# Kernel optimization log

Hardware: AMD Instinct MI355X
Metric: run time of the kernel (lower is better)

The kernel has to match this reference:

```python
import jax, jax.numpy as jnp
import numpy as np

# ---- static configuration (mirrors init_kwargs) ----
B, V, C, NH, HD = 1, 6, 256, 8, 32     # batch, views, embed, heads, head_dim
Z, L, P = 4, 4, 2                       # z-ref points, fmap levels, ref points
BEV_H, BEV_W = 80, 80
Q = BEV_H * BEV_W
IMG_H, IMG_W = 480, 800
LEVEL_SHAPES = [(60, 100), (30, 50), (15, 25), (8, 13)]
S = sum(h * w for h, w in LEVEL_SHAPES)
RES = 0.512
OFFSET_SCALE = 1.0
FF = 512


def layer_norm(x, g, b):
    m = jnp.mean(x, -1, keepdims=True)
    v = jnp.var(x, -1, keepdims=True)
    return (x - m) / jnp.sqrt(v + 1e-5) * g + b


def _bev_grid():
    xs = (jnp.arange(BEV_W) + 0.5) / BEV_W
    ys = (jnp.arange(BEV_H) + 0.5) / BEV_H
    gy, gx = jnp.meshgrid(ys, xs, indexing='ij')
    ref = jnp.stack([gx.reshape(-1), gy.reshape(-1)], -1)        # (Q,2) normalized xy
    world = (ref - 0.5) * jnp.array([BEV_W * RES, BEV_H * RES])  # (Q,2) ego-frame meters
    return ref, world


def deform_sample(value, H, W, loc):
    """Bilinear sampling. value: (N, H*W, NH, HD); loc: (N, Qn, NH, PP, 2) in [0,1].
    Returns (N, Qn, NH, PP, HD); out-of-bounds samples contribute zero."""
    v = jnp.moveaxis(value, 2, 1)                                # (N, NH, HW, HD)
    x = loc[..., 0] * W - 0.5
    y = loc[..., 1] * H - 0.5
    x0 = jnp.floor(x); y0 = jnp.floor(y)
    lx, ly = x - x0, y - y0
    x0 = x0.astype(jnp.int32); y0 = y0.astype(jnp.int32)
    gather = jax.vmap(jax.vmap(lambda vt, it: vt[it]))           # over (N, NH)
    def corner(xi, yi, w):
        ok = ((xi >= 0) & (xi < W) & (yi >= 0) & (yi < H)).astype(value.dtype)
        idx = jnp.clip(yi, 0, H - 1) * W + jnp.clip(xi, 0, W - 1)
        g = gather(v, jnp.moveaxis(idx, 2, 1))                   # (N,NH,Qn,PP,HD)
        return jnp.moveaxis(g, 1, 2) * (w * ok)[..., None]
    return (corner(x0, y0, (1 - lx) * (1 - ly)) + corner(x0 + 1, y0, lx * (1 - ly))
            + corner(x0, y0 + 1, (1 - lx) * ly) + corner(x0 + 1, y0 + 1, lx * ly))


def _forward(bev_queries, bev_histories, multiscale_fmaps, transition_matrices, z_refs,
             cam_proj_matrices, Wv_t, Woff_t, boff_t, Ww_t, bw_t, Wo_t, bo_t, ln1_g, ln1_b,
             Wv_s, Woff_s, boff_s, Ww_s, bw_s, Wo_s, bo_s, ln2_g, ln2_b,
             W1, b1, W2, b2, ln3_g, ln3_b):
    ref, world = _bev_grid()
    q = bev_queries
    # ---------- temporal self-attention (deformable over current + warped history) ----------
    vcur = (q @ Wv_t).reshape(B, Q, NH, HD)
    vhist = (bev_histories @ Wv_t).reshape(B, Q, NH, HD)
    off_t = (q @ Woff_t + boff_t).reshape(B, Q, NH, 2, P, 2) * OFFSET_SCALE
    w_t = jax.nn.softmax((q @ Ww_t + bw_t).reshape(B, Q, NH, 2 * P), -1).reshape(B, Q, NH, 2, P)
    ext = jnp.array([BEV_W * RES, BEV_H * RES], jnp.float32)
    wh = jnp.concatenate([world, jnp.ones((Q, 1), jnp.float32)], -1)     # (Q,3)
    warped = jnp.einsum('bij,qj->bqi', transition_matrices, wh)          # (B,Q,3)
    ref_hist = warped[..., :2] / warped[..., 2:3] / ext + 0.5            # (B,Q,2)
    norm_bev = jnp.array([BEV_W, BEV_H], jnp.float32)
    loc_c = ref[None, :, None, None, :] + off_t[:, :, :, 0] / norm_bev
    loc_h = ref_hist[:, :, None, None, :] + off_t[:, :, :, 1] / norm_bev
    s_c = deform_sample(vcur, BEV_H, BEV_W, loc_c)                       # (B,Q,NH,P,HD)
    s_h = deform_sample(vhist, BEV_H, BEV_W, loc_h)
    out_t = (jnp.einsum('bqhp,bqhpd->bqhd', w_t[:, :, :, 0], s_c)
             + jnp.einsum('bqhp,bqhpd->bqhd', w_t[:, :, :, 1], s_h))
    out1 = out_t.reshape(B, Q, C) @ Wo_t + bo_t
    out2 = layer_norm(out1 + q, ln1_g, ln1_b)
    # ---------- spatial cross-attention (multi-view multi-scale deformable) ----------
    val = (multiscale_fmaps @ Wv_s).reshape(B * V, S, NH, HD)
    pts = jnp.concatenate([
        jnp.broadcast_to(world[:, None, :], (Q, Z, 2)),
        jnp.broadcast_to(z_refs[None, :, None], (Q, Z, 1)),
        jnp.ones((Q, Z, 1), jnp.float32)], -1)                           # (Q,Z,4) homogeneous
    uvd = jnp.einsum('vij,qzj->vqzi', cam_proj_matrices, pts)            # (V,Q,Z,3)
    d = uvd[..., 2]
    un = uvd[..., 0] / jnp.maximum(d, 1e-5) / IMG_W
    vn = uvd[..., 1] / jnp.maximum(d, 1e-5) / IMG_H
    valid = ((d > 1e-5) & (un >= 0) & (un <= 1) & (vn >= 0) & (vn <= 1)).astype(q.dtype)
    refuv = jnp.stack([un, vn], -1)                                      # (V,Q,Z,2)
    off_s = (out2 @ Woff_s + boff_s).reshape(B, Q, NH, Z, L, P, 2) * OFFSET_SCALE
    w_s = jax.nn.softmax((out2 @ Ww_s + bw_s).reshape(B, Q, NH, Z * L * P), -1)
    w_s = w_s.reshape(B, Q, NH, Z, L, P)
    acc = jnp.zeros((B, Q, NH, HD), q.dtype)
    start = 0
    for l, (Hl, Wl) in enumerate(LEVEL_SHAPES):
        vl = val[:, start:start + Hl * Wl]
        start += Hl * Wl
        loc = (refuv[None, :, :, None, :, None, :]
               + off_s[:, None, :, :, :, l] / jnp.array([Wl, Hl], jnp.float32))
        loc = jnp.broadcast_to(loc, (B, V, Q, NH, Z, P, 2)).reshape(B * V, Q, NH, Z * P, 2)
        samp = deform_sample(vl, Hl, Wl, loc).reshape(B, V, Q, NH, Z, P, HD)
        wl = w_s[:, None, :, :, :, l] * valid[None, :, :, None, :, None]
        acc = acc + jnp.einsum('bvqhzp,bvqhzpd->bqhd', wl, samp)
    count = jnp.maximum(valid.sum((0, 2)), 1.0)                          # (Q,) hit count
    out3 = (acc / count[None, :, None, None]).reshape(B, Q, C) @ Wo_s + bo_s
    out4 = layer_norm(out3 + out2, ln2_g, ln2_b)
    # ---------- feed-forward ----------
    out5 = jax.nn.relu(out4 @ W1 + b1) @ W2 + b2
    return layer_norm(out5 + out4, ln3_g, ln3_b)


def setup_inputs() -> dict:
    key = jax.random.key(0)
    ks = iter(jax.random.split(key, 40))
    def rn(shape, s=1.0):
        return jax.random.normal(next(ks), shape, jnp.float32) * s
    sc = 1.0 / float(np.sqrt(C))
    inp = {}
    inp['bev_queries'] = rn((B, Q, C), 0.1)
    inp['bev_histories'] = rn((B, Q, C), 0.1)
    inp['multiscale_fmaps'] = rn((B, V, S, C), 0.1)
    th = 0.02
    T = np.array([[np.cos(th), -np.sin(th), 0.5],
                  [np.sin(th), np.cos(th), 0.1],
                  [0.0, 0.0, 1.0]], np.float32)
    inp['transition_matrices'] = jnp.tile(jnp.asarray(T)[None], (B, 1, 1))
    inp['z_refs'] = jnp.linspace(-5.0, 3.0, Z).astype(jnp.float32)
    K = np.array([[400.0, 0.0, IMG_W / 2], [0.0, 400.0, IMG_H / 2], [0.0, 0.0, 1.0]], np.float32)
    Ps = []
    for vi in range(V):
        a = 2 * np.pi * vi / V
        Rt = np.zeros((3, 4), np.float32)
        Rt[0, :3] = [-np.sin(a), np.cos(a), 0.0]   # camera right
        Rt[1, :3] = [0.0, 0.0, -1.0]               # camera down
        Rt[2, :3] = [np.cos(a), np.sin(a), 0.0]    # camera forward
        Ps.append(K @ Rt)
    inp['cam_proj_matrices'] = jnp.asarray(np.stack(Ps))
    # temporal self-attention params
    inp['Wv_t'] = rn((C, C), sc)
    inp['Woff_t'] = rn((C, NH * 2 * P * 2), sc * 0.1)
    inp['boff_t'] = jnp.zeros((NH * 2 * P * 2,), jnp.float32)
    inp['Ww_t'] = rn((C, NH * 2 * P), sc)
    inp['bw_t'] = jnp.zeros((NH * 2 * P,), jnp.float32)
    inp['Wo_t'] = rn((C, C), sc)
    inp['bo_t'] = jnp.zeros((C,), jnp.float32)
    inp['ln1_g'] = jnp.ones((C,), jnp.float32)
    inp['ln1_b'] = jnp.zeros((C,), jnp.float32)
    # spatial cross-attention params
    inp['Wv_s'] = rn((C, C), sc)
    inp['Woff_s'] = rn((C, NH * Z * L * P * 2), sc * 0.1)
    inp['boff_s'] = jnp.zeros((NH * Z * L * P * 2,), jnp.float32)
    inp['Ww_s'] = rn((C, NH * Z * L * P), sc)
    inp['bw_s'] = jnp.zeros((NH * Z * L * P,), jnp.float32)
    inp['Wo_s'] = rn((C, C), sc)
    inp['bo_s'] = jnp.zeros((C,), jnp.float32)
    inp['ln2_g'] = jnp.ones((C,), jnp.float32)
    inp['ln2_b'] = jnp.zeros((C,), jnp.float32)
    # FFN params
    inp['W1'] = rn((C, FF), sc)
    inp['b1'] = jnp.zeros((FF,), jnp.float32)
    inp['W2'] = rn((FF, C), 1.0 / float(np.sqrt(FF)))
    inp['b2'] = jnp.zeros((C,), jnp.float32)
    inp['ln3_g'] = jnp.ones((C,), jnp.float32)
    inp['ln3_b'] = jnp.zeros((C,), jnp.float32)
    # static shape descriptors (treated as compile-time constants)
    inp['bev_spatial_shape'] = np.array([[BEV_H, BEV_W]], np.int64)
    inp['multiscale_fmap_shapes'] = np.array(LEVEL_SHAPES, np.int64)
    inp['img_spatial_shape'] = np.array([[IMG_H, IMG_W]], np.int64)
    return inp


def reference(bev_queries, bev_histories, multiscale_fmaps, transition_matrices, z_refs,
              cam_proj_matrices, Wv_t, Woff_t, boff_t, Ww_t, bw_t, Wo_t, bo_t, ln1_g, ln1_b,
              Wv_s, Woff_s, boff_s, Ww_s, bw_s, Wo_s, bo_s, ln2_g, ln2_b,
              W1, b1, W2, b2, ln3_g, ln3_b,
              bev_spatial_shape, multiscale_fmap_shapes, img_spatial_shape):
    return _forward(bev_queries, bev_histories, multiscale_fmaps, transition_matrices, z_refs,
                    cam_proj_matrices, Wv_t, Woff_t, boff_t, Ww_t, bw_t, Wo_t, bo_t, ln1_g, ln1_b,
                    Wv_s, Woff_s, boff_s, Ww_s, bw_s, Wo_s, bo_s, ln2_g, ln2_b,
                    W1, b1, W2, b2, ln3_g, ln3_b)
```

## Files before the change

### kernel.cpp

```cpp
#include <hip/hip_runtime.h>
#include <hip/hip_bf16.h>
#include <hip/hip_fp16.h>

typedef unsigned short u16;
typedef unsigned int u32;
typedef __attribute__((ext_vector_type(8))) _Float16 f16x8;
typedef __attribute__((ext_vector_type(4))) float f32x4;

#define Q_N  6400
#define S_N  7979
#define BEV  80

__device__ __forceinline__ float f16tof(u16 u) {
    __half h; *(u16*)&h = u; return __half2float(h);
}
__device__ __forceinline__ u16 ftof16(float f) {
    __half h = __float2half(f); return *(u16*)&h;
}

template <int AIN, int RELU, int OUTMODE, int SM4, int SM32>
__device__ __forceinline__ void gemm_body(
    const void* __restrict__ A, const u16* __restrict__ WT,
    const float* __restrict__ bias, const float* __restrict__ bias2,
    void* __restrict__ Cout, int M, int N, int K, int bx, int by,
    u16* Ah, u16* Wh)
{
    const int tid  = threadIdx.x;
    const int lane = tid & 63;
    const int wave = tid >> 6;
    const int wm = (wave >> 1) * 32, wn = (wave & 1) * 64;
    const int m0 = by * 64, n0 = bx * 128;
    const int arow = tid >> 2, ak = (tid & 3) * 8;
    const int wrow = tid >> 1, wk = (tid & 1) * 16;
    const int fr = lane & 15, g = lane >> 4;

    f32x4 acc[8];
    #pragma unroll
    for (int i = 0; i < 8; ++i) acc[i] = (f32x4)(0.f);

    for (int k0 = 0; k0 < K; k0 += 32) {
        {
            const bool okr = (m0 + arow) < M;
            u16* dh = &Ah[arow * 40 + ak];
            if (AIN == 0) {
                const float* ap = (const float*)A + (size_t)(m0 + arow) * K + k0 + ak;
                float4 v0 = okr ? *(const float4*)(ap)     : make_float4(0.f, 0.f, 0.f, 0.f);
                float4 v1 = okr ? *(const float4*)(ap + 4) : make_float4(0.f, 0.f, 0.f, 0.f);
                u16 hb[8];
                hb[0] = ftof16(v0.x); hb[1] = ftof16(v0.y);
                hb[2] = ftof16(v0.z); hb[3] = ftof16(v0.w);
                hb[4] = ftof16(v1.x); hb[5] = ftof16(v1.y);
                hb[6] = ftof16(v1.z); hb[7] = ftof16(v1.w);
                *(ushort4*)(dh)     = *(ushort4*)&hb[0];
                *(ushort4*)(dh + 4) = *(ushort4*)&hb[4];
            } else {
                const u16* ap = (const u16*)A + (size_t)(m0 + arow) * K + k0 + ak;
                uint4 u = okr ? *(const uint4*)ap : make_uint4(0, 0, 0, 0);
                *(uint4*)dh = u;
            }
        }
        {
            const size_t wo = (size_t)(n0 + wrow) * K + k0 + wk;
            *(uint4*)&Wh[wrow * 40 + wk]     = *(const uint4*)(WT + wo);
            *(uint4*)&Wh[wrow * 40 + wk + 8] = *(const uint4*)(WT + wo + 8);
        }
        __syncthreads();
        f16x8 fah[2], fwh[4];
        #pragma unroll
        for (int i = 0; i < 2; ++i)
            fah[i] = *(const f16x8*)&Ah[(wm + i * 16 + fr) * 40 + g * 8];
        #pragma unroll
        for (int j = 0; j < 4; ++j)
            fwh[j] = *(const f16x8*)&Wh[(wn + j * 16 + fr) * 40 + g * 8];
        #pragma unroll
        for (int i = 0; i < 2; ++i)
            #pragma unroll
            for (int j = 0; j < 4; ++j)
                acc[i * 4 + j] = __builtin_amdgcn_mfma_f32_16x16x32_f16(fah[i], fwh[j], acc[i * 4 + j], 0, 0, 0);
        __syncthreads();
    }
    const int g4r = g * 4;
    float bv[4];
    #pragma unroll
    for (int j = 0; j < 4; ++j) {
        int col = n0 + wn + j * 16 + fr;
        if (bias2) bv[j] = (col < 512) ? bias[col] : bias2[col - 512];
        else       bv[j] = bias ? bias[col] : 0.f;
    }
    const bool do_sm4  = SM4 && (wn == 64);
    #pragma unroll
    for (int i = 0; i < 2; ++i) {
        #pragma unroll
        for (int r = 0; r < 4; ++r) {
            const int row = m0 + wm + i * 16 + g4r + r;
            float v0 = acc[i * 4 + 0][r] + bv[0];
            float v1 = acc[i * 4 + 1][r] + bv[1];
            float v2 = acc[i * 4 + 2][r] + bv[2];
            float v3 = acc[i * 4 + 3][r] + bv[3];
            if (RELU) {
                v0 = fmaxf(v0, 0.f); v1 = fmaxf(v1, 0.f);
                v2 = fmaxf(v2, 0.f); v3 = fmaxf(v3, 0.f);
            }
            if (SM4 && do_sm4) {
                float m0q = fmaxf(v0, __shfl_xor(v0, 1));
                m0q = fmaxf(m0q, __shfl_xor(m0q, 2));
                float e0 = __expf(v0 - m0q);
                float s0 = e0 + __shfl_xor(e0, 1);
                s0 += __shfl_xor(s0, 2);
                v0 = e0 / s0;
                float m1q = fmaxf(v1, __shfl_xor(v1, 1));
                m1q = fmaxf(m1q, __shfl_xor(m1q, 2));
                float e1 = __expf(v1 - m1q);
                float s1 = e1 + __shfl_xor(e1, 1);
                s1 += __shfl_xor(s1, 2);
                v1 = e1 / s1;
                v2 = 0.f; v3 = 0.f;
            }
            if (row < M) {
                const int colb = n0 + wn + fr;
                if (OUTMODE == 1) {
                    u16* cp = (u16*)Cout + (size_t)row * N;
                    cp[colb]      = ftof16(v0);
                    cp[colb + 16] = ftof16(v1);
                    cp[colb + 32] = ftof16(v2);
                    cp[colb + 48] = ftof16(v3);
                } else {
                    float* cp = (float*)Cout + (size_t)row * N;
                    cp[colb]      = v0;
                    cp[colb + 16] = v1;
                    cp[colb + 32] = v2;
                    cp[colb + 48] = v3;
                }
            }
        }
    }
}

__global__ __launch_bounds__(256) void fused3_k(
    const float* __restrict__ fmaps, const float* __restrict__ q, const float* __restrict__ hist,
    const u16* __restrict__ Wv_s_h, const u16* __restrict__ Wv_t_h,
    const u16* __restrict__ Wc_h, const float* __restrict__ bc,
    u16* __restrict__ val_f16, u16* __restrict__ vcur, u16* __restrict__ vhist,
    float* __restrict__ owt)
{
    __shared__ u16 Ah[64 * 40], Wh[128 * 40];
    const int b = blockIdx.x;
    if (b < 1498) {
        gemm_body<0, 0, 1, 0, 0>(fmaps, Wv_s_h, nullptr, nullptr, val_f16,
                                 47874, 256, 256, b & 1, b >> 1, Ah, Wh);
    } else if (b < 1698) {
        int l = b - 1498;
        gemm_body<0, 0, 1, 0, 0>(q, Wv_t_h, nullptr, nullptr, vcur,
                                 6400, 256, 256, l & 1, l >> 1, Ah, Wh);
    } else if (b < 1898) {
        int l = b - 1698;
        gemm_body<0, 0, 1, 0, 0>(hist, Wv_t_h, nullptr, nullptr, vhist,
                                 6400, 256, 256, l & 1, l >> 1, Ah, Wh);
    } else {
        int l = b - 1898;
        gemm_body<0, 0, 0, 1, 0>(q, Wc_h, bc, nullptr, owt,
                                 6400, 128, 256, 0, l, Ah, Wh);
    }
}

template <int AIN, int RELU, int OUTMODE, int SM32>
__global__ __launch_bounds__(256, 4) void cgemm_k(
    const void* __restrict__ A, const u16* __restrict__ WT,
    const float* __restrict__ bias, const float* __restrict__ bias2,
    void* __restrict__ Cout, int M, int N, int K)
{
    __shared__ u16 As[2][32 * 40];
    __shared__ u16 Wsh[2][64 * 40];
    const int tid  = threadIdx.x;
    const int lane = tid & 63;
    const int wave = tid >> 6;
    const int wm = (wave >> 1) * 16, wn = (wave & 1) * 32;
    const int fr = lane & 15, g = lane >> 4;
    const int nx = gridDim.x;
    const int nwg = nx * gridDim.y;
    const int o = blockIdx.y * nx + blockIdx.x;
    const int flat = (o & 7) * (nwg >> 3) + (o >> 3);
    const int bx = flat % nx, by = flat / nx;
    const int m0 = by * 32, n0 = bx * 64;
    const int ar = tid >> 3, ak = (tid & 7) * 4;
    const int wr = tid >> 2, wk = (tid & 3) * 8;
    const int NS = K >> 5;

    f32x4 acc[2] = {(f32x4)(0.f), (f32x4)(0.f)};

    const float* apf = (const float*)A + (size_t)(m0 + ar) * K + ak;
    const u16*  aph  = (const u16*)A + (size_t)(m0 + ar) * K + ak;
    const u16*  wp   = WT + (size_t)(n0 + wr) * K + wk;

    if (AIN == 0) {
        float4 v = *(const float4*)apf;
        u16 hb[4];
        hb[0] = ftof16(v.x); hb[1] = ftof16(v.y); hb[2] = ftof16(v.z); hb[3] = ftof16(v.w);
        *(ushort4*)&As[0][ar * 40 + ak] = *(ushort4*)&hb[0];
    } else {
        *(uint2*)&As[0][ar * 40 + ak] = *(const uint2*)aph;
    }
    *(uint4*)&Wsh[0][wr * 40 + wk] = *(const uint4*)wp;
    __syncthreads();

    for (int s = 0; s < NS; ++s) {
        float4 av; uint2 au; uint4 wv;
        const bool pf = (s + 1) < NS;
        if (pf) {
            if (AIN == 0) av = *(const float4*)(apf + (s + 1) * 32);
            else          au = *(const uint2*)(aph + (s + 1) * 32);
            wv = *(const uint4*)(wp + (s + 1) * 32);
        }
        const int b = s & 1;
        f16x8 fa  = *(const f16x8*)&As[b][(wm + fr) * 40 + g * 8];
        f16x8 fw0 = *(const f16x8*)&Wsh[b][(wn + fr) * 40 + g * 8];
        f16x8 fw1 = *(const f16x8*)&Wsh[b][(wn + 16 + fr) * 40 + g * 8];
        acc[0] = __builtin_amdgcn_mfma_f32_16x16x32_f16(fa, fw0, acc[0], 0, 0, 0);
        acc[1] = __builtin_amdgcn_mfma_f32_16x16x32_f16(fa, fw1, acc[1], 0, 0, 0);
        if (pf) {
            const int nb = b ^ 1;
            if (AIN == 0) {
                u16 hb[4];
                hb[0] = ftof16(av.x); hb[1] = ftof16(av.y);
                hb[2] = ftof16(av.z); hb[3] = ftof16(av.w);
                *(ushort4*)&As[nb][ar * 40 + ak] = *(ushort4*)&hb[0];
            } else {
                *(uint2*)&As[nb][ar * 40 + ak] = au;
            }
            *(uint4*)&Wsh[nb][wr * 40 + wk] = wv;
        }
        __syncthreads();
    }

    const int c0g = n0 + wn + fr, c1g = c0g + 16;
    float bv0, bv1;
    if (bias2) {
        bv0 = (c0g < 512) ? bias[c0g] : bias2[c0g - 512];
        bv1 = (c1g < 512) ? bias[c1g] : bias2[c1g - 512];
    } else {
        bv0 = bias ? bias[c0g] : 0.f;
        bv1 = bias ? bias[c1g] : 0.f;
    }
    const bool do_sm32 = SM32 && ((n0 + wn) >= 512);
    #pragma unroll
    for (int r = 0; r < 4; ++r) {
        const int row = m0 + wm + g * 4 + r;
        float v0 = acc[0][r] + bv0;
        float v1 = acc[1][r] + bv1;
        if (RELU) { v0 = fmaxf(v0, 0.f); v1 = fmaxf(v1, 0.f); }
        if (SM32 && do_sm32) {
            float ma = fmaxf(v0, v1);
            ma = fmaxf(ma, __shfl_xor(ma, 1));
            ma = fmaxf(ma, __shfl_xor(ma, 2));
            ma = fmaxf(ma, __shfl_xor(ma, 4));
            ma = fmaxf(ma, __shfl_xor(ma, 8));
            float e0 = __expf(v0 - ma), e1 = __expf(v1 - ma);
            float sa = e0 + e1;
            sa += __shfl_xor(sa, 1);
            sa += __shfl_xor(sa, 2);
            sa += __shfl_xor(sa, 4);
            sa += __shfl_xor(sa, 8);
            float ia = 1.f / sa;
            v0 = e0 * ia; v1 = e1 * ia;
        }
        if (row < M) {
            if (OUTMODE == 1) {
                u16* cp = (u16*)Cout + (size_t)row * N;
                cp[c0g] = ftof16(v0);
                cp[c1g] = ftof16(v1);
            } else {
                float* cp = (float*)Cout + (size_t)row * N;
                cp[c0g] = v0;
                cp[c1g] = v1;
            }
        }
    }
}

__global__ __launch_bounds__(256) void wprep_k(
    const float* __restrict__ w0, const float* __restrict__ w1, const float* __restrict__ w2,
    const float* __restrict__ w3, const float* __restrict__ w4, const float* __restrict__ w5,
    const float* __restrict__ w6, const float* __restrict__ w7, u16* __restrict__ base,
    const float* __restrict__ Woff_t, const float* __restrict__ Ww_t,
    const float* __restrict__ boff_t, const float* __restrict__ bw_t,
    float* __restrict__ bc)
{
    const int b = blockIdx.x, tid = threadIdx.x;
    if (b == 184) {
        if (tid < 128) bc[tid] = (tid < 64) ? boff_t[tid] : (tid < 96 ? bw_t[tid - 64] : 0.f);
        return;
    }
    const int cum[10]  = {0, 16, 32, 48, 80, 96, 112, 144, 176, 184};
    const int Ks[9]    = {256, 256, 256, 256, 256, 256, 256, 512, 256};
    const int Ns[9]    = {256, 256, 256, 512, 256, 256, 512, 256, 128};
    const int hoff[9]  = {0, 65536, 131072, 196608, 327680, 393216, 458752, 589824, 720896};
    int seg = 0;
    #pragma unroll
    for (int s = 1; s < 9; ++s) if (b >= cum[s]) seg = s;
    const int K = Ks[seg], N = Ns[seg];
    const int t = b - cum[seg];
    const int ntn = N / 64;
    const int k0 = (t / ntn) * 64, n0 = (t % ntn) * 64;
    __shared__ float tile[64][65];
    const int rr = tid >> 2, cc = (tid & 3) * 16;
    if (seg < 8) {
        const float* W = seg == 0 ? w0 : seg == 1 ? w1 : seg == 2 ? w2 : seg == 3 ? w3 :
                         seg == 4 ? w4 : seg == 5 ? w5 : seg == 6 ? w6 : w7;
        #pragma unroll
        for (int c = 0; c < 4; ++c) {
            float4 v = *(const float4*)(W + (size_t)(k0 + rr) * N + n0 + cc + c * 4);
            tile[rr][cc + c * 4 + 0] = v.x;
            tile[rr][cc + c * 4 + 1] = v.y;
            tile[rr][cc + c * 4 + 2] = v.z;
            tile[rr][cc + c * 4 + 3] = v.w;
        }
    } else {
        #pragma unroll
        for (int i = 0; i < 16; ++i) {
            int n = n0 + cc + i, k = k0 + rr;
            float v = (n < 64) ? Woff_t[k * 64 + n] : (n < 96 ? Ww_t[k * 32 + n - 64] : 0.f);
            tile[rr][cc + i] = v;
        }
    }
    __syncthreads();
    const int nr = tid >> 2, kc = (tid & 3) * 16;
    u16 hb[16];
    #pragma unroll
    for (int i = 0; i < 16; ++i) hb[i] = ftof16(tile[kc + i][nr]);
    u16* hp = base + hoff[seg] + (size_t)(n0 + nr) * K + k0 + kc;
    *(ushort4*)(hp + 0)  = *(ushort4*)&hb[0];
    *(ushort4*)(hp + 4)  = *(ushort4*)&hb[4];
    *(ushort4*)(hp + 8)  = *(ushort4*)&hb[8];
    *(ushort4*)(hp + 12) = *(ushort4*)&hb[12];
}

__global__ __launch_bounds__(256) void ln_k(
    const float* __restrict__ x, const float* __restrict__ res,
    const float* __restrict__ g, const float* __restrict__ b,
    float* __restrict__ out)
{
    const int row = blockIdx.x, t = threadIdx.x;
    const size_t idx = (size_t)row * 256 + t;
    float v = x[idx] + res[idx];
    float s = v, ss = v * v;
    #pragma unroll
    for (int o = 32; o > 0; o >>= 1) {
        s += __shfl_down(s, o);
        ss += __shfl_down(ss, o);
    }
    __shared__ float red[8];
    __shared__ float mv[2];
    const int wv = t >> 6, ln = t & 63;
    if (ln == 0) { red[wv] = s; red[4 + wv] = ss; }
    __syncthreads();
    if (t == 0) {
        float S = red[0] + red[1] + red[2] + red[3];
        float SS = red[4] + red[5] + red[6] + red[7];
        float mean = S * (1.f / 256.f);
        float var = SS * (1.f / 256.f) - mean * mean;
        mv[0] = mean;
        mv[1] = rsqrtf(var + 1e-5f);
    }
    __syncthreads();
    out[idx] = (v - mv[0]) * mv[1] * g[t] + b[t];
}

__device__ __forceinline__ float4 bilin4h(const u16* __restrict__ v, int H, int W,
                                          float x, float y, int chb)
{
    float xf = floorf(x), yf = floorf(y);
    int x0 = (int)xf, y0 = (int)yf;
    int x1 = x0 + 1, y1 = y0 + 1;
    float fx = x - xf, fy = y - yf;
    float w00 = (1.f - fx) * (1.f - fy), w10 = fx * (1.f - fy);
    float w01 = (1.f - fx) * fy,         w11 = fx * fy;
    bool xi0 = (x0 >= 0) && (x0 < W);
    bool xi1 = (x1 >= 0) && (x1 < W);
    bool yi0 = (y0 >= 0) && (y0 < H);
    bool yi1 = (y1 >= 0) && (y1 < H);
    float4 r = make_float4(0.f, 0.f, 0.f, 0.f);
    #define CORNER(xi, yi, xx, yy, ww)                                           \
        if ((yi) && (xi)) {                                                      \
            uint2 u = *(const uint2*)(v + ((size_t)(yy) * W + (xx)) * 256 + chb);\
            float2 f0 = __half22float2(*(const __half2*)&u.x);                   \
            float2 f1 = __half22float2(*(const __half2*)&u.y);                   \
            r.x += (ww) * f0.x; r.y += (ww) * f0.y;                              \
            r.z += (ww) * f1.x; r.w += (ww) * f1.y;                              \
        }
    CORNER(xi0, yi0, x0, y0, w00)
    CORNER(xi1, yi0, x1, y0, w10)
    CORNER(xi0, yi1, x0, y1, w01)
    CORNER(xi1, yi1, x1, y1, w11)
    #undef CORNER
    return r;
}

__global__ __launch_bounds__(256) void temporal_k(
    const u16* __restrict__ vcur, const u16* __restrict__ vhist,
    const float* __restrict__ ow,
    const float* __restrict__ Tm, float* __restrict__ outt)
{
    const int b = blockIdx.x;
    const int q = (b & 7) * 800 + (b >> 3);
    const int tid = threadIdx.x;
    const int c4 = tid & 63, rep = tid >> 6;
    const int br = rep >> 1, p = rep & 1;
    const int h = c4 >> 3;
    const int chb = h * 32 + (c4 & 7) * 4;
    const int jx = q % BEV, iy = q / BEV;
    const float refx = (jx + 0.5f) / 80.f;
    const float refy = (iy + 0.5f) / 80.f;
    const float wx = (refx - 0.5f) * 40.96f;
    const float wy = (refy - 0.5f) * 40.96f;
    float bx, by;
    const u16* v;
    if (br == 0) { v = vcur; bx = refx; by = refy; }
    else {
        float h0 = Tm[0] * wx + Tm[1] * wy + Tm[2];
        float h1 = Tm[3] * wx + Tm[4] * wy + Tm[5];
        float h2 = Tm[6] * wx + Tm[7] * wy + Tm[8];
        v = vhist;
        bx = h0 / h2 / 40.96f + 0.5f;
        by = h1 / h2 / 40.96f + 0.5f;
    }
    const float* owq = ow + (size_t)q * 128;
    int ob = h * 8 + br * 4 + p * 2;
    float lx = bx + owq[ob] * (1.f / 80.f);
    float ly = by + owq[ob + 1] * (1.f / 80.f);
    float wgt = owq[64 + h * 4 + br * 2 + p];
    float4 sv = bilin4h(v, BEV, BEV, lx * 80.f - 0.5f, ly * 80.f - 0.5f, chb);
    __shared__ float4 s_acc[4][64];
    s_acc[rep][c4] = make_float4(wgt * sv.x, wgt * sv.y, wgt * sv.z, wgt * sv.w);
    __syncthreads();
    if (rep == 0) {
        float4 a = s_acc[0][c4], b2 = s_acc[1][c4], c = s_acc[2][c4], d = s_acc[3][c4];
        float4 o = make_float4(a.x + b2.x + c.x + d.x, a.y + b2.y + c.y + d.y,
                               a.z + b2.z + c.z + d.z, a.w + b2.w + c.w + d.w);
        *(float4*)(outt + (size_t)q * 256 + c4 * 4) = o;
    }
}

__global__ __launch_bounds__(256) void spatial_k(
    const u16* __restrict__ val, const u16* __restrict__ ow,
    const float* __restrict__ cam, const float* __restrict__ zrefs,
    float* __restrict__ out)
{
    const int b = blockIdx.x;
    const int q = (b & 7) * 800 + (b >> 3);
    const int tid = threadIdx.x;
    const int lane = tid & 63, wave = tid >> 6;
    const int hw = lane >> 5, lh = lane & 31;
    const int slot = wave * 2 + hw;
    const int h = lh >> 2, chb = h * 32 + (lh & 3) * 8;
    __shared__ float s_un[24], s_vn[24], s_ok[24];
    __shared__ int s_list[24];
    __shared__ int s_n;
    __shared__ float s_cnt;
    __shared__ float s_ox[256], s_oy[256], s_wt[256];
    __shared__ float s_part[8][256];
    const int jx = q % BEV, iy = q / BEV;
    const float wx = ((jx + 0.5f) / 80.f - 0.5f) * 40.96f;
    const float wy = ((iy + 0.5f) / 80.f - 0.5f) * 40.96f;
    if (tid < 24) {
        int v = tid >> 2, zz = tid & 3;
        float zr = zrefs[zz];
        const float* P = cam + v * 12;
        float u0 = P[0] * wx + P[1] * wy + P[2] * zr + P[3];
        float u1 = P[4] * wx + P[5] * wy + P[6] * zr + P[7];
        float dd = P[8] * wx + P[9] * wy + P[10] * zr + P[11];
        float dm = fmaxf(dd, 1e-5f);
        float un = u0 / dm / 800.f;
        float vn = u1 / dm / 480.f;
        bool ok = (dd > 1e-5f) && (un >= 0.f) && (un <= 1.f) && (vn >= 0.f) && (vn <= 1.f);
        s_un[tid] = un; s_vn[tid] = vn; s_ok[tid] = ok ? 1.f : 0.f;
    }
    {
        const u16* owq = ow + (size_t)q * 768;
        #pragma unroll
        for (int rep = 0; rep < 2; ++rep) {
            int flat = tid + rep * 256;
            int hh = flat >> 6, rem = flat & 63;
            int zz = rem >> 4, ll = (rem >> 2) & 3, pp = (rem >> 1) & 1, xy = rem & 1;
            int dst = (zz * 8 + ll * 2 + pp) * 8 + hh;
            float v = f16tof(owq[flat]);
            if (xy) s_oy[dst] = v; else s_ox[dst] = v;
        }
        int hh = tid >> 5, rem = tid & 31;
        s_wt[rem * 8 + hh] = f16tof(owq[512 + tid]);
    }
    __syncthreads();
    if (tid == 0) {
        int n = 0; float c = 0.f;
        for (int vz = 0; vz < 24; ++vz) {
            if (s_ok[vz] != 0.f) { s_list[n++] = vz; c += 1.f; }
        }
        s_n = n; s_cnt = fmaxf(c, 1.f);
    }
    __syncthreads();
    const int n4 = s_n * 4;
    float a0 = 0.f, a1 = 0.f, a2 = 0.f, a3 = 0.f, a4 = 0.f, a5 = 0.f, a6 = 0.f, a7 = 0.f;
    for (int w = slot; w < n4; w += 8) {
        const int it = w >> 2, l = w & 3;
        const int vz = s_list[it];
        const int v = vz >> 2, z = vz & 3;
        const float un = s_un[vz], vn = s_vn[vz];
        const int Hl  = (l == 0) ? 60  : (l == 1) ? 30   : (l == 2) ? 15   : 8;
        const int Wl  = (l == 0) ? 100 : (l == 1) ? 50   : (l == 2) ? 25   : 13;
        const int LSo = (l == 0) ? 0   : (l == 1) ? 6000 : (l == 2) ? 7500 : 7875;
        const u16* lv = val + ((size_t)v * S_N + LSo) * 256 + chb;
        const float unl = un * Wl - 0.5f, vnl = vn * Hl - 0.5f;
        const int Ws = Wl * 256;
        #pragma unroll
        for (int p = 0; p < 2; ++p) {
            const int idx = (z * 8 + l * 2 + p) * 8 + h;
            float x = unl + s_ox[idx];
            float y = vnl + s_oy[idx];
            float wgt = s_wt[idx];
            float xf = floorf(x), yf = floorf(y);
            int x0 = (int)xf, y0 = (int)yf;
            float fx = x - xf, fy = y - yf;
            bool xi0 = (x0 >= 0) & (x0 < Wl);
            bool xi1 = (x0 >= -1) & (x0 < Wl - 1);
            bool yi0 = (y0 >= 0) & (y0 < Hl);
            bool yi1 = (y0 >= -1) & (y0 < Hl - 1);
            int xc0 = min(max(x0, 0), Wl - 1);
            int xc1 = min(max(x0 + 1, 0), Wl - 1);
            int yc0 = min(max(y0, 0), Hl - 1);
            int yc1 = min(max(y0 + 1, 0), Hl - 1);
            float m00 = (xi0 & yi0) ? wgt : 0.f;
            float m10 = (xi1 & yi0) ? wgt : 0.f;
            float m01 = (xi0 & yi1) ? wgt : 0.f;
            float m11 = (xi1 & yi1) ? wgt : 0.f;
            __half2 w00 = __float2half2_rn((1.f - fx) * (1.f - fy) * m00);
            __half2 w10 = __float2half2_rn(fx * (1.f - fy) * m10);
            __half2 w01 = __float2half2_rn((1.f - fx) * fy * m01);
            __half2 w11 = __float2half2_rn(fx * fy * m11);
            const u16* r0p = lv + (size_t)yc0 * Ws;
            const u16* r1p = lv + (size_t)yc1 * Ws;
            uint4 u00 = *(const uint4*)(r0p + (size_t)xc0 * 256);
            uint4 u10 = *(const uint4*)(r0p + (size_t)xc1 * 256);
            uint4 u01 = *(const uint4*)(r1p + (size_t)xc0 * 256);
            uint4 u11 = *(const uint4*)(r1p + (size_t)xc1 * 256);
            __half2 h0 = __float2half2_rn(0.f), h1 = h0, h2 = h0, h3 = h0;
            {
                const __half2* hp = (const __half2*)&u00;
                h0 = __hfma2(w00, hp[0], h0); h1 = __hfma2(w00, hp[1], h1);
                h2 = __hfma2(w00, hp[2], h2); h3 = __hfma2(w00, hp[3], h3);
            }
            {
                const __half2* hp = (const __half2*)&u10;
                h0 = __hfma2(w10, hp[0], h0); h1 = __hfma2(w10, hp[1], h1);
                h2 = __hfma2(w10, hp[2], h2); h3 = __hfma2(w10, hp[3], h3);
            }
            {
                const __half2* hp = (const __half2*)&u01;
                h0 = __hfma2(w01, hp[0], h0); h1 = __hfma2(w01, hp[1], h1);
                h2 = __hfma2(w01, hp[2], h2); h3 = __hfma2(w01, hp[3], h3);
            }
            {
                const __half2* hp = (const __half2*)&u11;
                h0 = __hfma2(w11, hp[0], h0); h1 = __hfma2(w11, hp[1], h1);
                h2 = __hfma2(w11, hp[2], h2); h3 = __hfma2(w11, hp[3], h3);
            }
            float2 f0 = __half22float2(h0), f1 = __half22float2(h1);
            float2 f2 = __half22float2(h2), f3 = __half22float2(h3);
            a0 += f0.x; a1 += f0.y; a2 += f1.x; a3 += f1.y;
            a4 += f2.x; a5 += f2.y; a6 += f3.x; a7 += f3.y;
        }
    }
    *(float4*)&s_part[slot][chb]     = make_float4(a0, a1, a2, a3);
    *(float4*)&s_part[slot][chb + 4] = make_float4(a4, a5, a6, a7);
    __syncthreads();
    float sum = 0.f;
    #pragma unroll
    for (int k = 0; k < 8; ++k) sum += s_part[k][tid];
    out[(size_t)q * 256 + tid] = sum / s_cnt;
}

extern "C" void kernel_launch(void* const* d_in, const int* in_sizes, int n_in,
                              void* d_out, int out_size, void* d_ws, size_t ws_size,
                              hipStream_t stream) {
    (void)in_sizes; (void)n_in; (void)out_size; (void)ws_size;
    const float* q      = (const float*)d_in[0];
    const float* hist   = (const float*)d_in[1];
    const float* fmaps  = (const float*)d_in[2];
    const float* Tm     = (const float*)d_in[3];
    const float* zrefs  = (const float*)d_in[4];
    const float* cam    = (const float*)d_in[5];
    const float* Woff_t = (const float*)d_in[7];
    const float* boff_t = (const float*)d_in[8];
    const float* Ww_t   = (const float*)d_in[9];
    const float* bw_t   = (const float*)d_in[10];
    const float* bo_t   = (const float*)d_in[12];
    const float* ln1g   = (const float*)d_in[13];
    const float* ln1b   = (const float*)d_in[14];
    const float* boff_s = (const float*)d_in[17];
    const float* bw_s   = (const float*)d_in[19];
    const float* bo_s   = (const float*)d_in[21];
    const float* ln2g   = (const float*)d_in[22];
    const float* ln2b   = (const float*)d_in[23];
    const float* b1     = (const float*)d_in[25];
    const float* b2     = (const float*)d_in[27];
    const float* ln3g   = (const float*)d_in[28];
    const float* ln3b   = (const float*)d_in[29];

    float* ws    = (float*)d_ws;
    float* r0    = ws;
    float* r1    = ws + 1638400;
    float* owt   = ws + 3276800;
    float* r4    = ws + 4096000;
    u16*  r5u    = (u16*)(ws + 5734400);
    float* of4   = ws + 8192000;
    u16*  valbuf = (u16*)(ws + 9830400);
    u16*  vcur   = (u16*)(ws + 15958272);
    u16*  vhist  = (u16*)(ws + 16777472);
    u16*  wtab   = (u16*)(ws + 17596672);
    float* bc    = ws + 18350336;

    u16* hidden = valbuf;
    u16* Wv_t_h = wtab + 0;
    u16* Wo_t_h = wtab + 65536;
    u16* Wv_s_h = wtab + 131072;
    u16* Comb_h = wtab + 196608;
    u16* Wo_s_h = wtab + 393216;
    u16* W1_h   = wtab + 458752;
    u16* W2_h   = wtab + 589824;
    u16* Wc_h   = wtab + 720896;

    dim3 blk(256);
    auto gc = [](int M, int N) { return dim3((unsigned)(N / 64), (unsigned)((M + 31) / 32)); };

    wprep_k<<<dim3(185), blk, 0, stream>>>(
        (const float*)d_in[6], (const float*)d_in[11], (const float*)d_in[15],
        (const float*)d_in[16], (const float*)d_in[18], (const float*)d_in[20],
        (const float*)d_in[24], (const float*)d_in[26], wtab,
        Woff_t, Ww_t, boff_t, bw_t, bc);
    fused3_k<<<dim3(1998), blk, 0, stream>>>(
        fmaps, q, hist, Wv_s_h, Wv_t_h, Wc_h, bc,
        valbuf, vcur, vhist, owt);
    temporal_k<<<dim3(6400), blk, 0, stream>>>(vcur, vhist, owt, Tm, r4);
    cgemm_k<0,0,0,0><<<gc(6400, 256), blk, 0, stream>>>(
        r4, Wo_t_h, bo_t, nullptr, r0, 6400, 256, 256);
    ln_k<<<dim3(6400), blk, 0, stream>>>(r0, q, ln1g, ln1b, r1);
    cgemm_k<0,0,1,1><<<gc(6400, 768), blk, 0, stream>>>(
        r1, Comb_h, boff_s, bw_s, r5u, 6400, 768, 256);
    spatial_k<<<dim3(6400), blk, 0, stream>>>(valbuf, r5u, cam, zrefs, r0);
    cgemm_k<0,0,0,0><<<gc(6400, 256), blk, 0, stream>>>(
        r0, Wo_s_h, bo_s, nullptr, r4, 6400, 256, 256);
    ln_k<<<dim3(6400), blk, 0, stream>>>(r4, r1, ln2g, ln2b, of4);
    cgemm_k<0,1,1,0><<<gc(6400, 512), blk, 0, stream>>>(
        of4, W1_h, b1, nullptr, hidden, 6400, 512, 256);
    cgemm_k<1,0,0,0><<<gc(6400, 256), blk, 0, stream>>>(
        hidden, W2_h, b2, nullptr, r0, 6400, 256, 512);
    ln_k<<<dim3(6400), blk, 0, stream>>>(r0, of4, ln3g, ln3b, (float*)d_out);
}
```

Measured before the change: 304.4 us.

## Double-buffer GEMM LDS tiles and widen spatial sampling per-thread channels

```diff
diff --git a/kernel.cpp b/kernel.cpp
--- a/kernel.cpp
+++ b/kernel.cpp
@@ -33,50 +33,85 @@
     const int arow = tid >> 2, ak = (tid & 3) * 8;
     const int wrow = tid >> 1, wk = (tid & 1) * 16;
     const int fr = lane & 15, g = lane >> 4;
+    const int NS = K >> 5;
+
+    const bool okr = (m0 + arow) < M;
+    const float* apf = (const float*)A + (size_t)(m0 + arow) * K + ak;
+    const u16*  aph  = (const u16*)A + (size_t)(m0 + arow) * K + ak;
+    const u16*  wp   = WT + (size_t)(n0 + wrow) * K + wk;
 
     f32x4 acc[8];
     #pragma unroll
     for (int i = 0; i < 8; ++i) acc[i] = (f32x4)(0.f);
 
-    for (int k0 = 0; k0 < K; k0 += 32) {
-        {
-            const bool okr = (m0 + arow) < M;
-            u16* dh = &Ah[arow * 40 + ak];
+    {
+        u16* dh = &Ah[arow * 40 + ak];
+        if (AIN == 0) {
+            float4 v0 = okr ? *(const float4*)(apf)     : make_float4(0.f, 0.f, 0.f, 0.f);
+            float4 v1 = okr ? *(const float4*)(apf + 4) : make_float4(0.f, 0.f, 0.f, 0.f);
+            u16 hb[8];
+            hb[0] = ftof16(v0.x); hb[1] = ftof16(v0.y);
+            hb[2] = ftof16(v0.z); hb[3] = ftof16(v0.w);
+            hb[4] = ftof16(v1.x); hb[5] = ftof16(v1.y);
+            hb[6] = ftof16(v1.z); hb[7] = ftof16(v1.w);
+            *(ushort4*)(dh)     = *(ushort4*)&hb[0];
+            *(ushort4*)(dh + 4) = *(ushort4*)&hb[4];
+        } else {
+            uint4 u = okr ? *(const uint4*)aph : make_uint4(0, 0, 0, 0);
+            *(uint4*)dh = u;
+        }
+        *(uint4*)&Wh[wrow * 40 + wk]     = *(const uint4*)(wp);
+        *(uint4*)&Wh[wrow * 40 + wk + 8] = *(const uint4*)(wp + 8);
+    }
+    __syncthreads();
+
+    for (int s = 0; s < NS; ++s) {
+        float4 av0, av1; uint4 au; uint4 wv0, wv1;
+        const bool pf = (s + 1) < NS;
+        if (pf) {
             if (AIN == 0) {
-                const float* ap = (const float*)A + (size_t)(m0 + arow) * K + k0 + ak;
-                float4 v0 = okr ? *(const float4*)(ap)     : make_float4(0.f, 0.f, 0.f, 0.f);
-                float4 v1 = okr ? *(const float4*)(ap + 4) : make_float4(0.f, 0.f, 0.f, 0.f);
-                u16 hb[8];
-                hb[0] = ftof16(v0.x); hb[1] = ftof16(v0.y);
-                hb[2] = ftof16(v0.z); hb[3] = ftof16(v0.w);
-                hb[4] = ftof16(v1.x); hb[5] = ftof16(v1.y);
-                hb[6] = ftof16(v1.z); hb[7] = ftof16(v1.w);
-                *(ushort4*)(dh)     = *(ushort4*)&hb[0];
-                *(ushort4*)(dh + 4) = *(ushort4*)&hb[4];
+                av0 = okr ? *(const float4*)(apf + (s + 1) * 32)     : make_float4(0.f, 0.f, 0.f, 0.f);
+                av1 = okr ? *(const float4*)(apf + (s + 1) * 32 + 4) : make_float4(0.f, 0.f, 0.f, 0.f);
             } else {
-                const u16* ap = (const u16*)A + (size_t)(m0 + arow) * K + k0 + ak;
-                uint4 u = okr ? *(const uint4*)ap : make_uint4(0, 0, 0, 0);
-                *(uint4*)dh = u;
-            }
-        }
-        {
-            const size_t wo = (size_t)(n0 + wrow) * K + k0 + wk;
-            *(uint4*)&Wh[wrow * 40 + wk]     = *(const uint4*)(WT + wo);
-            *(uint4*)&Wh[wrow * 40 + wk + 8] = *(const uint4*)(WT + wo + 8);
-        }
-        __syncthreads();
+                au = okr ? *(const uint4*)(aph + (s + 1) * 32) : make_uint4(0, 0, 0, 0);
+            }
+            wv0 = *(const uint4*)(wp + (s + 1) * 32);
+            wv1 = *(const uint4*)(wp + (s + 1) * 32 + 8);
+        }
+        const int b = s & 1;
+        const u16* Ab = Ah + b * 2560;
+        const u16* Wb = Wh + b * 5120;
         f16x8 fah[2], fwh[4];
         #pragma unroll
         for (int i = 0; i < 2; ++i)
-            fah[i] = *(const f16x8*)&Ah[(wm + i * 16 + fr) * 40 + g * 8];
+            fah[i] = *(const f16x8*)&Ab[(wm + i * 16 + fr) * 40 + g * 8];
         #pragma unroll
         for (int j = 0; j < 4; ++j)
-            fwh[j] = *(const f16x8*)&Wh[(wn + j * 16 + fr) * 40 + g * 8];
+            fwh[j] = *(const f16x8*)&Wb[(wn + j * 16 + fr) * 40 + g * 8];
         #pragma unroll
         for (int i = 0; i < 2; ++i)
             #pragma unroll
             for (int j = 0; j < 4; ++j)
                 acc[i * 4 + j] = __builtin_amdgcn_mfma_f32_16x16x32_f16(fah[i], fwh[j], acc[i * 4 + j], 0, 0, 0);
+        if (pf) {
+            const int nb = b ^ 1;
+            u16* Anb = Ah + nb * 2560;
+            u16* Wnb = Wh + nb * 5120;
+            u16* dh = &Anb[arow * 40 + ak];
+            if (AIN == 0) {
+                u16 hb[8];
+                hb[0] = ftof16(av0.x); hb[1] = ftof16(av0.y);
+                hb[2] = ftof16(av0.z); hb[3] = ftof16(av0.w);
+                hb[4] = ftof16(av1.x); hb[5] = ftof16(av1.y);
+                hb[6] = ftof16(av1.z); hb[7] = ftof16(av1.w);
+                *(ushort4*)(dh)     = *(ushort4*)&hb[0];
+                *(ushort4*)(dh + 4) = *(ushort4*)&hb[4];
+            } else {
+                *(uint4*)dh = au;
+            }
+            *(uint4*)&Wnb[wrow * 40 + wk]     = wv0;
+            *(uint4*)&Wnb[wrow * 40 + wk + 8] = wv1;
+        }
         __syncthreads();
     }
     const int g4r = g * 4;
@@ -143,7 +178,7 @@
     u16* __restrict__ val_f16, u16* __restrict__ vcur, u16* __restrict__ vhist,
     float* __restrict__ owt)
 {
-    __shared__ u16 Ah[64 * 40], Wh[128 * 40];
+    __shared__ u16 Ah[2 * 64 * 40], Wh[2 * 128 * 40];
     const int b = blockIdx.x;
     if (b < 1498) {
         gemm_body<0, 0, 1, 0, 0>(fmaps, Wv_s_h, nullptr, nullptr, val_f16,
@@ -449,15 +484,15 @@
     const int q = (b & 7) * 800 + (b >> 3);
     const int tid = threadIdx.x;
     const int lane = tid & 63, wave = tid >> 6;
-    const int hw = lane >> 5, lh = lane & 31;
-    const int slot = wave * 2 + hw;
-    const int h = lh >> 2, chb = h * 32 + (lh & 3) * 8;
+    const int qw = lane >> 4, lh = lane & 15;
+    const int slot = wave * 4 + qw;
+    const int h = lh >> 1, chb = h * 32 + (lh & 1) * 16;
     __shared__ float s_un[24], s_vn[24], s_ok[24];
     __shared__ int s_list[24];
     __shared__ int s_n;
     __shared__ float s_cnt;
     __shared__ float s_ox[256], s_oy[256], s_wt[256];
-    __shared__ float s_part[8][256];
+    __shared__ float s_part[16][256];
     const int jx = q % BEV, iy = q / BEV;
     const float wx = ((jx + 0.5f) / 80.f - 0.5f) * 40.96f;
     const float wy = ((iy + 0.5f) / 80.f - 0.5f) * 40.96f;
@@ -498,8 +533,10 @@
     }
     __syncthreads();
     const int n4 = s_n * 4;
-    float a0 = 0.f, a1 = 0.f, a2 = 0.f, a3 = 0.f, a4 = 0.f, a5 = 0.f, a6 = 0.f, a7 = 0.f;
-    for (int w = slot; w < n4; w += 8) {
+    float acc[16];
+    #pragma unroll
+    for (int i = 0; i < 16; ++i) acc[i] = 0.f;
+    for (int w = slot; w < n4; w += 16) {
         const int it = w >> 2, l = w & 3;
         const int vz = s_list[it];
         const int v = vz >> 2, z = vz & 3;
@@ -537,43 +574,73 @@
             __half2 w11 = __float2half2_rn(fx * fy * m11);
             const u16* r0p = lv + (size_t)yc0 * Ws;
             const u16* r1p = lv + (size_t)yc1 * Ws;
-            uint4 u00 = *(const uint4*)(r0p + (size_t)xc0 * 256);
-            uint4 u10 = *(const uint4*)(r0p + (size_t)xc1 * 256);
-            uint4 u01 = *(const uint4*)(r1p + (size_t)xc0 * 256);
-            uint4 u11 = *(const uint4*)(r1p + (size_t)xc1 * 256);
-            __half2 h0 = __float2half2_rn(0.f), h1 = h0, h2 = h0, h3 = h0;
+            const u16* c00 = r0p + (size_t)xc0 * 256;
+            const u16* c10 = r0p + (size_t)xc1 * 256;
+            const u16* c01 = r1p + (size_t)xc0 * 256;
+            const u16* c11 = r1p + (size_t)xc1 * 256;
+            uint4 a00 = *(const uint4*)(c00);
+            uint4 b00 = *(const uint4*)(c00 + 8);
+            uint4 a10 = *(const uint4*)(c10);
+            uint4 b10 = *(const uint4*)(c10 + 8);
+            uint4 a01 = *(const uint4*)(c01);
+            uint4 b01 = *(const uint4*)(c01 + 8);
+            uint4 a11 = *(const uint4*)(c11);
+            uint4 b11 = *(const uint4*)(c11 + 8);
+            __half2 t[8];
+            #pragma unroll
+            for (int i = 0; i < 8; ++i) t[i] = __float2half2_rn(0.f);
             {
-                const __half2* hp = (const __half2*)&u00;
-                h0 = __hfma2(w00, hp[0], h0); h1 = __hfma2(w00, hp[1], h1);
-                h2 = __hfma2(w00, hp[2], h2); h3 = __hfma2(w00, hp[3], h3);
+                const __half2* hp = (const __half2*)&a00;
+                const __half2* hq = (const __half2*)&b00;
+                #pragma unroll
+                for (int i = 0; i < 4; ++i) {
+                    t[i]     = __hfma2(w00, hp[i], t[i]);
+                    t[i + 4] = __hfma2(w00, hq[i], t[i + 4]);
+                }
             }
             {
-                const __half2* hp = (const __half2*)&u10;
-                h0 = __hfma2(w10, hp[0], h0); h1 = __hfma2(w10, hp[1], h1);
-                h2 = __hfma2(w10, hp[2], h2); h3 = __hfma2(w10, hp[3], h3);
+                const __half2* hp = (const __half2*)&a10;
+                const __half2* hq = (const __half2*)&b10;
+                #pragma unroll
+                for (int i = 0; i < 4; ++i) {
+                    t[i]     = __hfma2(w10, hp[i], t[i]);
+                    t[i + 4] = __hfma2(w10, hq[i], t[i + 4]);
+                }
             }
             {
-                const __half2* hp = (const __half2*)&u01;
-                h0 = __hfma2(w01, hp[0], h0); h1 = __hfma2(w01, hp[1], h1);
-                h2 = __hfma2(w01, hp[2], h2); h3 = __hfma2(w01, hp[3], h3);
+                const __half2* hp = (const __half2*)&a01;
+                const __half2* hq = (const __half2*)&b01;
+                #pragma unroll
+                for (int i = 0; i < 4; ++i) {
+                    t[i]     = __hfma2(w01, hp[i], t[i]);
+                    t[i + 4] = __hfma2(w01, hq[i], t[i + 4]);
+                }
             }
             {
-                const __half2* hp = (const __half2*)&u11;
-                h0 = __hfma2(w11, hp[0], h0); h1 = __hfma2(w11, hp[1], h1);
-                h2 = __hfma2(w11, hp[2], h2); h3 = __hfma2(w11, hp[3], h3);
-            }
-            float2 f0 = __half22float2(h0), f1 = __half22float2(h1);
-            float2 f2 = __half22float2(h2), f3 = __half22float2(h3);
-            a0 += f0.x; a1 += f0.y; a2 += f1.x; a3 += f1.y;
-            a4 += f2.x; a5 += f2.y; a6 += f3.x; a7 += f3.y;
-        }
-    }
-    *(float4*)&s_part[slot][chb]     = make_float4(a0, a1, a2, a3);
-    *(float4*)&s_part[slot][chb + 4] = make_float4(a4, a5, a6, a7);
+                const __half2* hp = (const __half2*)&a11;
+                const __half2* hq = (const __half2*)&b11;
+                #pragma unroll
+                for (int i = 0; i < 4; ++i) {
+                    t[i]     = __hfma2(w11, hp[i], t[i]);
+                    t[i + 4] = __hfma2(w11, hq[i], t[i + 4]);
+                }
+            }
+            #pragma unroll
+            for (int i = 0; i < 8; ++i) {
+                float2 f = __half22float2(t[i]);
+                acc[i * 2]     += f.x;
+                acc[i * 2 + 1] += f.y;
+            }
+        }
+    }
+    #pragma unroll
+    for (int i = 0; i < 4; ++i)
+        *(float4*)&s_part[slot][chb + i * 4] =
+            make_float4(acc[i * 4], acc[i * 4 + 1], acc[i * 4 + 2], acc[i * 4 + 3]);
     __syncthreads();
     float sum = 0.f;
     #pragma unroll
-    for (int k = 0; k < 8; ++k) sum += s_part[k][tid];
+    for (int k = 0; k < 16; ++k) sum += s_part[k][tid];
     out[(size_t)q * 256 + tid] = sum / s_cnt;
 }
 
```

Measured after the change: 310.2 us. About the same (+1.9%).

## Fuse residual LayerNorms into adjacent GEMMs via atomic row statistics

Applied to the files above, without the earlier changes.

```diff
diff --git a/kernel.cpp b/kernel.cpp
--- a/kernel.cpp
+++ b/kernel.cpp
@@ -163,10 +163,13 @@
     }
 }
 
-template <int AIN, int RELU, int OUTMODE, int SM32>
+template <int AIN, int RELU, int OUTMODE, int SM32, int STATS, int LNA>
 __global__ __launch_bounds__(256, 4) void cgemm_k(
     const void* __restrict__ A, const u16* __restrict__ WT,
     const float* __restrict__ bias, const float* __restrict__ bias2,
+    const float* __restrict__ res, float* __restrict__ rstat,
+    const float* __restrict__ lng, const float* __restrict__ lnb,
+    float* __restrict__ aux,
     void* __restrict__ Cout, int M, int N, int K)
 {
     __shared__ u16 As[2][32 * 40];
@@ -192,8 +195,30 @@
     const u16*  aph  = (const u16*)A + (size_t)(m0 + ar) * K + ak;
     const u16*  wp   = WT + (size_t)(n0 + wr) * K + wk;
 
+    const float* rp = nullptr;
+    float* auxp = nullptr;
+    float mean = 0.f, rstd = 0.f;
+    if (LNA) {
+        rp = res + (size_t)(m0 + ar) * 256 + ak;
+        if (bx == 0) auxp = aux + (size_t)(m0 + ar) * 256 + ak;
+        const float sm = rstat[m0 + ar];
+        const float sq = rstat[Q_N + m0 + ar];
+        mean = sm * (1.f / 256.f);
+        rstd = rsqrtf(sq * (1.f / 256.f) - mean * mean + 1e-5f);
+    }
+
     if (AIN == 0) {
         float4 v = *(const float4*)apf;
+        if (LNA) {
+            float4 rr = *(const float4*)rp;
+            float4 gg = *(const float4*)(lng + ak);
+            float4 bb = *(const float4*)(lnb + ak);
+            v.x = (v.x + rr.x - mean) * rstd * gg.x + bb.x;
+            v.y = (v.y + rr.y - mean) * rstd * gg.y + bb.y;
+            v.z = (v.z + rr.z - mean) * rstd * gg.z + bb.z;
+            v.w = (v.w + rr.w - mean) * rstd * gg.w + bb.w;
+            if (auxp) *(float4*)auxp = v;
+        }
         u16 hb[4];
         hb[0] = ftof16(v.x); hb[1] = ftof16(v.y); hb[2] = ftof16(v.z); hb[3] = ftof16(v.w);
         *(ushort4*)&As[0][ar * 40 + ak] = *(ushort4*)&hb[0];
@@ -204,11 +229,15 @@
     __syncthreads();
 
     for (int s = 0; s < NS; ++s) {
-        float4 av; uint2 au; uint4 wv;
+        float4 av; float4 rv; uint2 au; uint4 wv;
         const bool pf = (s + 1) < NS;
         if (pf) {
-            if (AIN == 0) av = *(const float4*)(apf + (s + 1) * 32);
-            else          au = *(const uint2*)(aph + (s + 1) * 32);
+            if (AIN == 0) {
+                av = *(const float4*)(apf + (s + 1) * 32);
+                if (LNA) rv = *(const float4*)(rp + (s + 1) * 32);
+            } else {
+                au = *(const uint2*)(aph + (s + 1) * 32);
+            }
             wv = *(const uint4*)(wp + (s + 1) * 32);
         }
         const int b = s & 1;
@@ -220,6 +249,16 @@
         if (pf) {
             const int nb = b ^ 1;
             if (AIN == 0) {
+                if (LNA) {
+                    const int ko = ak + (s + 1) * 32;
+                    float4 gg = *(const float4*)(lng + ko);
+                    float4 bb = *(const float4*)(lnb + ko);
+                    av.x = (av.x + rv.x - mean) * rstd * gg.x + bb.x;
+                    av.y = (av.y + rv.y - mean) * rstd * gg.y + bb.y;
+                    av.z = (av.z + rv.z - mean) * rstd * gg.z + bb.z;
+                    av.w = (av.w + rv.w - mean) * rstd * gg.w + bb.w;
+                    if (auxp) *(float4*)(auxp + (s + 1) * 32) = av;
+                }
                 u16 hb[4];
                 hb[0] = ftof16(av.x); hb[1] = ftof16(av.y);
                 hb[2] = ftof16(av.z); hb[3] = ftof16(av.w);
@@ -263,6 +302,20 @@
             float ia = 1.f / sa;
             v0 = e0 * ia; v1 = e1 * ia;
         }
+        if (STATS) {
+            float t0 = v0 + res[(size_t)row * 256 + c0g];
+            float t1 = v1 + res[(size_t)row * 256 + c1g];
+            float s1v = t0 + t1;
+            float s2v = t0 * t0 + t1 * t1;
+            s1v += __shfl_xor(s1v, 1); s1v += __shfl_xor(s1v, 2);
+            s1v += __shfl_xor(s1v, 4); s1v += __shfl_xor(s1v, 8);
+            s2v += __shfl_xor(s2v, 1); s2v += __shfl_xor(s2v, 2);
+            s2v += __shfl_xor(s2v, 4); s2v += __shfl_xor(s2v, 8);
+            if (fr == 0) {
+                atomicAdd(&rstat[row], s1v);
+                atomicAdd(&rstat[Q_N + row], s2v);
+            }
+        }
         if (row < M) {
             if (OUTMODE == 1) {
                 u16* cp = (u16*)Cout + (size_t)row * N;
@@ -283,9 +336,13 @@
     const float* __restrict__ w6, const float* __restrict__ w7, u16* __restrict__ base,
     const float* __restrict__ Woff_t, const float* __restrict__ Ww_t,
     const float* __restrict__ boff_t, const float* __restrict__ bw_t,
-    float* __restrict__ bc)
+    float* __restrict__ bc, float* __restrict__ st)
 {
     const int b = blockIdx.x, tid = threadIdx.x;
+    if (b >= 185) {
+        st[(b - 185) * 256 + tid] = 0.f;
+        return;
+    }
     if (b == 184) {
         if (tid < 128) bc[tid] = (tid < 64) ? boff_t[tid] : (tid < 96 ? bw_t[tid - 64] : 0.f);
         return;
@@ -615,6 +672,8 @@
     u16*  vcur   = (u16*)(ws + 15958272);
     u16*  vhist  = (u16*)(ws + 16777472);
     u16*  wtab   = (u16*)(ws + 17596672);
+    float* st1   = ws + 17973504;
+    float* st2   = ws + 17986304;
     float* bc    = ws + 18350336;
 
     u16* hidden = valbuf;
@@ -630,27 +689,30 @@
     dim3 blk(256);
     auto gc = [](int M, int N) { return dim3((unsigned)(N / 64), (unsigned)((M + 31) / 32)); };
 
-    wprep_k<<<dim3(185), blk, 0, stream>>>(
+    wprep_k<<<dim3(285), blk, 0, stream>>>(
         (const float*)d_in[6], (const float*)d_in[11], (const float*)d_in[15],
         (const float*)d_in[16], (const float*)d_in[18], (const float*)d_in[20],
         (const float*)d_in[24], (const float*)d_in[26], wtab,
-        Woff_t, Ww_t, boff_t, bw_t, bc);
+        Woff_t, Ww_t, boff_t, bw_t, bc, st1);
     fused3_k<<<dim3(1998), blk, 0, stream>>>(
         fmaps, q, hist, Wv_s_h, Wv_t_h, Wc_h, bc,
         valbuf, vcur, vhist, owt);
     temporal_k<<<dim3(6400), blk, 0, stream>>>(vcur, vhist, owt, Tm, r4);
-    cgemm_k<0,0,0,0><<<gc(6400, 256), blk, 0, stream>>>(
-        r4, Wo_t_h, bo_t, nullptr, r0, 6400, 256, 256);
-    ln_k<<<dim3(6400), blk, 0, stream>>>(r0, q, ln1g, ln1b, r1);
-    cgemm_k<0,0,1,1><<<gc(6400, 768), blk, 0, stream>>>(
-        r1, Comb_h, boff_s, bw_s, r5u, 6400, 768, 256);
+    cgemm_k<0,0,0,0,1,0><<<gc(6400, 256), blk, 0, stream>>>(
+        r4, Wo_t_h, bo_t, nullptr, q, st1, nullptr, nullptr, nullptr,
+        r0, 6400, 256, 256);
+    cgemm_k<0,0,1,1,0,1><<<gc(6400, 768), blk, 0, stream>>>(
+        r0, Comb_h, boff_s, bw_s, q, st1, ln1g, ln1b, r1,
+        r5u, 6400, 768, 256);
     spatial_k<<<dim3(6400), blk, 0, stream>>>(valbuf, r5u, cam, zrefs, r0);
-    cgemm_k<0,0,0,0><<<gc(6400, 256), blk, 0, stream>>>(
-        r0, Wo_s_h, bo_s, nullptr, r4, 6400, 256, 256);
-    ln_k<<<dim3(6400), blk, 0, stream>>>(r4, r1, ln2g, ln2b, of4);
-    cgemm_k<0,1,1,0><<<gc(6400, 512), blk, 0, stream>>>(
-        of4, W1_h, b1, nullptr, hidden, 6400, 512, 256);
-    cgemm_k<1,0,0,0><<<gc(6400, 256), blk, 0, stream>>>(
-        hidden, W2_h, b2, nullptr, r0, 6400, 256, 512);
+    cgemm_k<0,0,0,0,1,0><<<gc(6400, 256), blk, 0, stream>>>(
+        r0, Wo_s_h, bo_s, nullptr, r1, st2, nullptr, nullptr, nullptr,
+        r4, 6400, 256, 256);
+    cgemm_k<0,1,1,0,0,1><<<gc(6400, 512), blk, 0, stream>>>(
+        r4, W1_h, b1, nullptr, r1, st2, ln2g, ln2b, of4,
+        hidden, 6400, 512, 256);
+    cgemm_k<1,0,0,0,0,0><<<gc(6400, 256), blk, 0, stream>>>(
+        hidden, W2_h, b2, nullptr, nullptr, nullptr, nullptr, nullptr, nullptr,
+        r0, 6400, 256, 512);
     ln_k<<<dim3(6400), blk, 0, stream>>>(r0, of4, ln3g, ln3b, (float*)d_out);
 }
```

After: 302.8 us. Within noise of the previous version (-0.5%).
